# Optimization experiments

Hardware: AMD Instinct MI355X
Metric: run time of the kernel (lower is better)

The kernel has to match this reference:

```python
import jax, jax.numpy as jnp
import numpy as np

B, S, D, H = 2, 2048, 1024, 16
DK = D // H  # 64
THETA = 10000.0


def setup_inputs() -> dict:
    key = jax.random.key(0)
    ks = jax.random.split(key, 5)
    scale = 1.0 / np.sqrt(D)
    return {
        "x": jax.random.normal(ks[0], (B, S, D), dtype=jnp.float32),
        "Wq": jax.random.normal(ks[1], (D, D), dtype=jnp.float32) * scale,
        "Wk": jax.random.normal(ks[2], (D, D), dtype=jnp.float32) * scale,
        "Wv": jax.random.normal(ks[3], (D, D), dtype=jnp.float32) * scale,
        "Wo": jax.random.normal(ks[4], (D, D), dtype=jnp.float32) * scale,
    }


def _rope(t):
    # t: (B, H, S, DK); interleaved-pair rotary embedding with positions 0..S-1
    s = t.shape[-2]
    inv_freq = 1.0 / (THETA ** (jnp.arange(0, DK, 2, dtype=jnp.float32) / DK))  # (DK/2,)
    ang = jnp.arange(s, dtype=jnp.float32)[:, None] * inv_freq[None, :]  # (S, DK/2)
    cos, sin = jnp.cos(ang), jnp.sin(ang)
    x1 = t[..., 0::2]
    x2 = t[..., 1::2]
    r1 = x1 * cos - x2 * sin
    r2 = x1 * sin + x2 * cos
    return jnp.stack([r1, r2], axis=-1).reshape(t.shape)


def reference(x, Wq, Wk, Wv, Wo):
    # Projections (Linear: y = x @ W^T), split heads -> (B, H, S, DK)
    def proj(W):
        y = jnp.einsum('bsd,ed->bse', x, W)
        return y.reshape(B, S, H, DK).transpose(0, 2, 1, 3)

    Q = _rope(proj(Wq))
    K = _rope(proj(Wk))
    V = proj(Wv)

    scores = jnp.einsum('bhqd,bhkd->bhqk', Q, K)
    scores = jnp.clip(scores, -80.0, 80.0)
    causal = jnp.tril(jnp.ones((S, S), dtype=bool))  # (S, S)
    scores = jnp.where(causal, scores, -jnp.inf)
    weights = jax.nn.softmax(scores / np.sqrt(DK), axis=-1)
    att = jnp.einsum('bhqk,bhkd->bhqd', weights, V)
    att = att.transpose(0, 2, 1, 3).reshape(B, S, D)
    return jnp.einsum('bsd,ed->bse', att, Wo)
```

## Files before the change

### kernel.cpp

```cpp
#include <hip/hip_runtime.h>
#include <hip/hip_bf16.h>

#define B_  2
#define S_  2048
#define D_  1024
#define H_  16
#define DK_ 64
#define BH_ (B_*H_)
#define M_  (B_*S_)

typedef __attribute__((ext_vector_type(8))) short bf16x8;
typedef __attribute__((ext_vector_type(4))) float f32x4;

__device__ inline float bf2f(unsigned short u) {
    return __uint_as_float(((unsigned)u) << 16);
}
__device__ inline unsigned short f2bf(float f) {
    unsigned u = __float_as_uint(f);
    u += 0x7fffu + ((u >> 16) & 1u);
    return (unsigned short)(u >> 16);
}
__device__ inline unsigned short f2bf_hw(float f) {
    __hip_bfloat16 h = __float2bfloat16(f);
    return *reinterpret_cast<unsigned short*>(&h);
}
__device__ inline unsigned packbf2(float lo, float hi) {
    return (unsigned)f2bf_hw(lo) | ((unsigned)f2bf_hw(hi) << 16);
}

__device__ inline void gld16(const void* g, void* l) {
    __builtin_amdgcn_global_load_lds(
        (const __attribute__((address_space(1))) unsigned int*)g,
        (__attribute__((address_space(3))) unsigned int*)l, 16, 0, 0);
}

__global__ void cast_f32_to_bf16(const float* __restrict__ src,
                                 unsigned short* __restrict__ dst, int n) {
    int i = (blockIdx.x * blockDim.x + threadIdx.x) * 4;
    int stride = gridDim.x * blockDim.x * 4;
    for (int j = i; j < n; j += stride) {
        float4 v = *reinterpret_cast<const float4*>(src + j);
        ushort4 o;
        o.x = f2bf(v.x); o.y = f2bf(v.y); o.z = f2bf(v.z); o.w = f2bf(v.w);
        *reinterpret_cast<ushort4*>(dst + j) = o;
    }
}

__global__ void cast4_f32_to_bf16(const float* __restrict__ s0, const float* __restrict__ s1,
                                  const float* __restrict__ s2, const float* __restrict__ s3,
                                  unsigned short* __restrict__ d0, unsigned short* __restrict__ d1,
                                  unsigned short* __restrict__ d2, unsigned short* __restrict__ d3) {
    const float* s; unsigned short* d;
    switch (blockIdx.y) {
        case 0: s = s0; d = d0; break;
        case 1: s = s1; d = d1; break;
        case 2: s = s2; d = d2; break;
        default: s = s3; d = d3; break;
    }
    int j = (blockIdx.x * blockDim.x + threadIdx.x) * 4;
    float4 v = *reinterpret_cast<const float4*>(s + j);
    ushort4 o;
    o.x = f2bf(v.x); o.y = f2bf(v.y); o.z = f2bf(v.z); o.w = f2bf(v.w);
    *reinterpret_cast<ushort4*>(d + j) = o;
}

#define BM 64
#define BN 128
#define BKG 64

__global__ __launch_bounds__(256)
void gemm_qkv(const unsigned short* __restrict__ A, const unsigned short* __restrict__ Wcat,
              unsigned short* __restrict__ Qw, unsigned short* __restrict__ Kw,
              unsigned short* __restrict__ Vt) {
    __shared__ unsigned short As[BM * BKG];
    __shared__ unsigned short Bs[BN * BKG];
    const int K = D_;
    const int tid  = threadIdx.x;
    const int lane = tid & 63;
    const int wid  = tid >> 6;
    const int wm = wid & 1, wn = wid >> 1;
    const int m0 = blockIdx.y * BM, n0 = blockIdx.x * BN;
    const int g  = lane >> 4, cl = lane & 15;

    f32x4 acc[2][4];
#pragma unroll
    for (int i = 0; i < 2; i++)
#pragma unroll
        for (int j = 0; j < 4; j++) acc[i][j] = f32x4{0.f, 0.f, 0.f, 0.f};

    const int srow = tid >> 3;
    const unsigned short* Asrc[2];
    const unsigned short* Bsrc[4];
#pragma unroll
    for (int q = 0; q < 2; q++) {
        int row = srow + q * 32;
        Asrc[q] = A + (long)(m0 + row) * K + (((tid & 7) ^ (row & 7)) * 8);
    }
#pragma unroll
    for (int q = 0; q < 4; q++) {
        int row = srow + q * 32;
        Bsrc[q] = Wcat + (long)(n0 + row) * K + (((tid & 7) ^ (row & 7)) * 8);
    }

    for (int k0 = 0; k0 < K; k0 += BKG) {
        __syncthreads();
#pragma unroll
        for (int q = 0; q < 2; q++) gld16(Asrc[q] + k0, As + tid * 8 + q * 2048);
#pragma unroll
        for (int q = 0; q < 4; q++) gld16(Bsrc[q] + k0, Bs + tid * 8 + q * 2048);
        __syncthreads();

#pragma unroll
        for (int kk = 0; kk < 2; kk++) {
            bf16x8 af[2], bfr[4];
#pragma unroll
            for (int i = 0; i < 2; i++) {
                int row = wm*32 + i*16 + cl;
                af[i]  = *reinterpret_cast<const bf16x8*>(As + row * BKG + (((kk*4 + g) ^ (cl & 7)) * 8));
            }
#pragma unroll
            for (int j = 0; j < 4; j++) {
                int row = wn*64 + j*16 + cl;
                bfr[j] = *reinterpret_cast<const bf16x8*>(Bs + row * BKG + (((kk*4 + g) ^ (cl & 7)) * 8));
            }
#pragma unroll
            for (int i = 0; i < 2; i++)
#pragma unroll
                for (int j = 0; j < 4; j++)
                    acc[i][j] = __builtin_amdgcn_mfma_f32_16x16x32_bf16(af[i], bfr[j], acc[i][j], 0, 0, 0);
        }
    }

    const int mat = n0 >> 10;
    if (mat < 2) {
        unsigned short* dst = mat ? Kw : Qw;
        float invf[4];
#pragma unroll
        for (int jj = 0; jj < 4; jj++)
            invf[jj] = exp2f(-(float)(jj*8 + (cl >> 1)) * 0.4152410118569779f);
#pragma unroll
        for (int i = 0; i < 2; i++) {
#pragma unroll
            for (int jj = 0; jj < 4; jj++) {
                const int gcl = (n0 & 1023) + wn*64 + jj*16 + cl;
                const int hh = gcl >> 6;
                const int dk = jj*16 + cl;
#pragma unroll
                for (int rr = 0; rr < 4; rr++) {
                    int gr = m0 + wm*32 + i*16 + g*4 + rr;
                    int bb = gr >> 11, s = gr & (S_ - 1);
                    float v = acc[i][jj][rr];
                    float p = __shfl_xor(v, 1);
                    float ang = (float)s * invf[jj];
                    float sn = __sinf(ang), cs = __cosf(ang);
                    float r = (cl & 1) ? fmaf(v, cs, p * sn) : fmaf(v, cs, -p * sn);
                    dst[(((long)(bb*H_ + hh) * S_ + s) << 6) + dk] = f2bf_hw(r);
                }
            }
        }
    } else {
#pragma unroll
        for (int i = 0; i < 2; i++) {
#pragma unroll
            for (int jj = 0; jj < 4; jj++) {
                const int gcl = (n0 & 1023) + wn*64 + jj*16 + cl;
                const int hh = gcl >> 6;
                const int dk = jj*16 + cl;
#pragma unroll
                for (int rr = 0; rr < 4; rr++) {
                    int gr = m0 + wm*32 + i*16 + g*4 + rr;
                    int bb = gr >> 11, s = gr & (S_ - 1);
                    Vt[((long)(bb*H_ + hh) * DK_ + dk) * S_ + s] = f2bf_hw(acc[i][jj][rr]);
                }
            }
        }
    }
}

__global__ __launch_bounds__(256)
void gemm_out(const unsigned short* __restrict__ A, const unsigned short* __restrict__ Bw,
              float* __restrict__ Cf) {
    __shared__ unsigned short As[BM * BKG];
    __shared__ unsigned short Bs[BN * BKG];
    const int K = D_;
    const int tid  = threadIdx.x;
    const int lane = tid & 63;
    const int wid  = tid >> 6;
    const int wm = wid & 1, wn = wid >> 1;
    const int m0 = blockIdx.y * BM, n0 = blockIdx.x * BN;
    const int g  = lane >> 4, cl = lane & 15;

    f32x4 acc[2][4];
#pragma unroll
    for (int i = 0; i < 2; i++)
#pragma unroll
        for (int j = 0; j < 4; j++) acc[i][j] = f32x4{0.f, 0.f, 0.f, 0.f};

    const int srow = tid >> 3;
    const unsigned short* Asrc[2];
    const unsigned short* Bsrc[4];
#pragma unroll
    for (int q = 0; q < 2; q++) {
        int row = srow + q * 32;
        Asrc[q] = A + (long)(m0 + row) * K + (((tid & 7) ^ (row & 7)) * 8);
    }
#pragma unroll
    for (int q = 0; q < 4; q++) {
        int row = srow + q * 32;
        Bsrc[q] = Bw + (long)(n0 + row) * K + (((tid & 7) ^ (row & 7)) * 8);
    }

    for (int k0 = 0; k0 < K; k0 += BKG) {
        __syncthreads();
#pragma unroll
        for (int q = 0; q < 2; q++) gld16(Asrc[q] + k0, As + tid * 8 + q * 2048);
#pragma unroll
        for (int q = 0; q < 4; q++) gld16(Bsrc[q] + k0, Bs + tid * 8 + q * 2048);
        __syncthreads();

#pragma unroll
        for (int kk = 0; kk < 2; kk++) {
            bf16x8 af[2], bfr[4];
#pragma unroll
            for (int i = 0; i < 2; i++) {
                int row = wm*32 + i*16 + cl;
                af[i]  = *reinterpret_cast<const bf16x8*>(As + row * BKG + (((kk*4 + g) ^ (cl & 7)) * 8));
            }
#pragma unroll
            for (int j = 0; j < 4; j++) {
                int row = wn*64 + j*16 + cl;
                bfr[j] = *reinterpret_cast<const bf16x8*>(Bs + row * BKG + (((kk*4 + g) ^ (cl & 7)) * 8));
            }
#pragma unroll
            for (int i = 0; i < 2; i++)
#pragma unroll
                for (int j = 0; j < 4; j++)
                    acc[i][j] = __builtin_amdgcn_mfma_f32_16x16x32_bf16(af[i], bfr[j], acc[i][j], 0, 0, 0);
        }
    }

#pragma unroll
    for (int i = 0; i < 2; i++)
#pragma unroll
        for (int j = 0; j < 4; j++)
#pragma unroll
            for (int rr = 0; rr < 4; rr++) {
                int gr = m0 + wm*32 + i*16 + g*4 + rr;
                int gc = n0 + wn*64 + j*16 + cl;
                Cf[(long)gr * D_ + gc] = acc[i][j][rr];
            }
}

#define WQ    32
#define KVBLK 64
#define LDP   72

__global__ __launch_bounds__(256)
void flash_attn(const unsigned short* __restrict__ Qw, const unsigned short* __restrict__ Kw,
                const unsigned short* __restrict__ Vt, unsigned short* __restrict__ Att) {
    __shared__ __align__(16) char smem[20480];
    const int tid  = threadIdx.x;
    const int lane = tid & 63;
    const int wid  = tid >> 6;
    const int g = lane >> 4, cl = lane & 15;
    const int bh = blockIdx.x & (BH_ - 1);
    const int pr = blockIdx.x >> 5;
    const int b = bh >> 4, h = bh & (H_ - 1);

    unsigned short* Ps = reinterpret_cast<unsigned short*>(smem) + wid * (WQ * LDP);
    f32x4* Ol = reinterpret_cast<f32x4*>(smem);
    float* Ll = reinterpret_cast<float*>(smem + 16384);

    const unsigned short* Kb = Kw + (long)bh * S_ * DK_;
    const unsigned short* Vb = Vt + (long)bh * DK_ * S_;

    for (int half = 0; half < 2; half++) {
        const int qt = half ? (S_/WQ - 1 - pr) : pr;
        const int q0 = qt * WQ;
        const int nt = (q0 + WQ + KVBLK - 1) / KVBLK;

        const unsigned short* Qb = Qw + ((long)bh * S_ + q0) * DK_;
        bf16x8 aq[2][2];
#pragma unroll
        for (int m = 0; m < 2; m++)
#pragma unroll
            for (int c = 0; c < 2; c++)
                aq[m][c] = *reinterpret_cast<const bf16x8*>(Qb + (m*16 + cl) * DK_ + c*32 + g*8);

        f32x4 o[2][4];
#pragma unroll
        for (int m = 0; m < 2; m++)
#pragma unroll
            for (int t = 0; t < 4; t++) o[m][t] = f32x4{0.f, 0.f, 0.f, 0.f};
        float lp[2] = {0.f, 0.f};

        for (int j = wid; j < nt; j += 4) {
            const int kv0 = j * KVBLK;
            bf16x8 bk[4][2];
#pragma unroll
            for (int n = 0; n < 4; n++)
#pragma unroll
                for (int c = 0; c < 2; c++)
                    bk[n][c] = *reinterpret_cast<const bf16x8*>(Kb + (long)(kv0 + n*16 + cl) * DK_ + c*32 + g*8);
            f32x4 sc[2][4];
#pragma unroll
            for (int m = 0; m < 2; m++)
#pragma unroll
                for (int n = 0; n < 4; n++) {
                    f32x4 z = f32x4{0.f, 0.f, 0.f, 0.f};
                    z = __builtin_amdgcn_mfma_f32_16x16x32_bf16(bk[n][0], aq[m][0], z, 0, 0, 0);
                    z = __builtin_amdgcn_mfma_f32_16x16x32_bf16(bk[n][1], aq[m][1], z, 0, 0, 0);
                    sc[m][n] = z;
                }

            if (kv0 + KVBLK - 1 > q0) {
#pragma unroll
                for (int m = 0; m < 2; m++) {
                    const int q = q0 + m*16 + cl;
#pragma unroll
                    for (int n = 0; n < 4; n++) {
                        float p4[4];
#pragma unroll
                        for (int rr = 0; rr < 4; rr++) {
                            float u = fminf(fmaf(sc[m][n][rr], 0.125f, -10.f), 0.f);
                            if (kv0 + n*16 + g*4 + rr > q) u = -1e30f;
                            p4[rr] = __expf(u);
                        }
                        lp[m] += (p4[0] + p4[1]) + (p4[2] + p4[3]);
                        *reinterpret_cast<uint2*>(Ps + (m*16 + cl) * LDP + n*16 + g*4)
                            = uint2{packbf2(p4[0], p4[1]), packbf2(p4[2], p4[3])};
                    }
                }
            } else {
#pragma unroll
                for (int m = 0; m < 2; m++) {
#pragma unroll
                    for (int n = 0; n < 4; n++) {
                        float p4[4];
#pragma unroll
                        for (int rr = 0; rr < 4; rr++)
                            p4[rr] = __expf(fminf(fmaf(sc[m][n][rr], 0.125f, -10.f), 0.f));
                        lp[m] += (p4[0] + p4[1]) + (p4[2] + p4[3]);
                        *reinterpret_cast<uint2*>(Ps + (m*16 + cl) * LDP + n*16 + g*4)
                            = uint2{packbf2(p4[0], p4[1]), packbf2(p4[2], p4[3])};
                    }
                }
            }

            bf16x8 pa[2][2];
#pragma unroll
            for (int m = 0; m < 2; m++)
#pragma unroll
                for (int c = 0; c < 2; c++)
                    pa[m][c] = *reinterpret_cast<const bf16x8*>(Ps + (m*16 + cl) * LDP + c*32 + g*8);
            bf16x8 bv[4][2];
#pragma unroll
            for (int t = 0; t < 4; t++)
#pragma unroll
                for (int c = 0; c < 2; c++)
                    bv[t][c] = *reinterpret_cast<const bf16x8*>(Vb + (long)(t*16 + cl) * S_ + kv0 + c*32 + g*8);
#pragma unroll
            for (int m = 0; m < 2; m++)
#pragma unroll
                for (int t = 0; t < 4; t++) {
                    o[m][t] = __builtin_amdgcn_mfma_f32_16x16x32_bf16(pa[m][0], bv[t][0], o[m][t], 0, 0, 0);
                    o[m][t] = __builtin_amdgcn_mfma_f32_16x16x32_bf16(pa[m][1], bv[t][1], o[m][t], 0, 0, 0);
                }
        }

        __syncthreads();
        if (wid == 1 || wid == 3) {
            const int slot = wid >> 1;
#pragma unroll
            for (int m = 0; m < 2; m++) {
#pragma unroll
                for (int t = 0; t < 4; t++)
                    Ol[(slot*8 + m*4 + t)*64 + lane] = o[m][t];
                Ll[(slot*2 + m)*64 + lane] = lp[m];
            }
        }
        __syncthreads();
        if (wid == 0 || wid == 2) {
            const int slot = wid >> 1;
#pragma unroll
            for (int m = 0; m < 2; m++) {
#pragma unroll
                for (int t = 0; t < 4; t++) {
                    f32x4 v = Ol[(slot*8 + m*4 + t)*64 + lane];
#pragma unroll
                    for (int rr = 0; rr < 4; rr++) o[m][t][rr] += v[rr];
                }
                lp[m] += Ll[(slot*2 + m)*64 + lane];
            }
        }
        __syncthreads();
        if (wid == 2) {
#pragma unroll
            for (int m = 0; m < 2; m++) {
#pragma unroll
                for (int t = 0; t < 4; t++)
                    Ol[(m*4 + t)*64 + lane] = o[m][t];
                Ll[m*64 + lane] = lp[m];
            }
        }
        __syncthreads();
        if (wid == 0) {
#pragma unroll
            for (int m = 0; m < 2; m++) {
#pragma unroll
                for (int t = 0; t < 4; t++) {
                    f32x4 v = Ol[(m*4 + t)*64 + lane];
#pragma unroll
                    for (int rr = 0; rr < 4; rr++) o[m][t][rr] += v[rr];
                }
                lp[m] += Ll[m*64 + lane];
                lp[m] += __shfl_xor(lp[m], 16);
                lp[m] += __shfl_xor(lp[m], 32);
            }
            float linv[2][4];
#pragma unroll
            for (int m = 0; m < 2; m++)
#pragma unroll
                for (int rr = 0; rr < 4; rr++)
                    linv[m][rr] = 1.0f / __shfl(lp[m], g*4 + rr);
#pragma unroll
            for (int m = 0; m < 2; m++)
#pragma unroll
                for (int t = 0; t < 4; t++)
#pragma unroll
                    for (int rr = 0; rr < 4; rr++) {
                        const int q = q0 + m*16 + g*4 + rr;
                        const int d = t*16 + cl;
                        Att[(long)(b * S_ + q) * D_ + h * DK_ + d] = f2bf_hw(o[m][t][rr] * linv[m][rr]);
                    }
        }
        __syncthreads();
    }
}

extern "C" void kernel_launch(void* const* d_in, const int* in_sizes, int n_in,
                              void* d_out, int out_size, void* d_ws, size_t ws_size,
                              hipStream_t stream) {
    const float* x  = (const float*)d_in[0];
    const float* Wq = (const float*)d_in[1];
    const float* Wk = (const float*)d_in[2];
    const float* Wv = (const float*)d_in[3];
    const float* Wo = (const float*)d_in[4];
    float* out = (float*)d_out;

    char* ws = (char*)d_ws;
    unsigned short* xb  = (unsigned short*)(ws);
    unsigned short* att = xb;
    unsigned short* WqB = (unsigned short*)(ws + (8  << 20));
    unsigned short* WkB = (unsigned short*)(ws + (10 << 20));
    unsigned short* WvB = (unsigned short*)(ws + (12 << 20));
    unsigned short* WoB = (unsigned short*)(ws + (14 << 20));
    unsigned short* Qw  = (unsigned short*)(ws + (16 << 20));
    unsigned short* Kw  = (unsigned short*)(ws + (24 << 20));
    unsigned short* Vt  = (unsigned short*)(ws + (32 << 20));

    const int nx = B_ * S_ * D_;
    cast_f32_to_bf16<<<4096, 256, 0, stream>>>(x, xb, nx);
    cast4_f32_to_bf16<<<dim3(1024, 4), 256, 0, stream>>>(Wq, Wk, Wv, Wo, WqB, WkB, WvB, WoB);

    dim3 qkvgrid(3 * D_ / BN, M_ / BM);
    gemm_qkv<<<qkvgrid, 256, 0, stream>>>(xb, WqB, Qw, Kw, Vt);

    flash_attn<<<(S_/WQ/2) * BH_, 256, 0, stream>>>(Qw, Kw, Vt, att);

    dim3 ogrid(D_ / BN, M_ / BM);
    gemm_out<<<ogrid, 256, 0, stream>>>(att, WoB, out);
}
```

Before: 144.3 us.

## Store Q/K/V in MFMA fragment-native layout for contiguous attention loads

The QKV GEMM epilogue now writes Q, K and V into a pre-swizzled layout matching the MFMA operand fragment order, so each lane in flash attention loads its 16-byte fragment from a contiguous wave-wide 1KB block. Before, K and Q loads were strided by rows and V loads were strided by S. V stores are also vectorized to ushort4 instead of scalar transposed writes. The cost is more complex index math in the producer and scattered scalar stores for Q/K.

```diff
diff --git a/kernel.cpp b/kernel.cpp
--- a/kernel.cpp
+++ b/kernel.cpp
@@ -70,8 +70,8 @@
 
 __global__ __launch_bounds__(256)
 void gemm_qkv(const unsigned short* __restrict__ A, const unsigned short* __restrict__ Wcat,
-              unsigned short* __restrict__ Qw, unsigned short* __restrict__ Kw,
-              unsigned short* __restrict__ Vt) {
+              unsigned short* __restrict__ Qf, unsigned short* __restrict__ Kf,
+              unsigned short* __restrict__ Vf) {
     __shared__ unsigned short As[BM * BKG];
     __shared__ unsigned short Bs[BN * BKG];
     const int K = D_;
@@ -133,7 +133,7 @@
 
     const int mat = n0 >> 10;
     if (mat < 2) {
-        unsigned short* dst = mat ? Kw : Qw;
+        unsigned short* dst = mat ? Kf : Qf;
         float invf[4];
 #pragma unroll
         for (int jj = 0; jj < 4; jj++)
@@ -145,6 +145,9 @@
                 const int gcl = (n0 & 1023) + wn*64 + jj*16 + cl;
                 const int hh = gcl >> 6;
                 const int dk = jj*16 + cl;
+                const int c  = dk >> 5;
+                const int lsel = ((dk >> 3) & 3) << 4;
+                const int e  = dk & 7;
 #pragma unroll
                 for (int rr = 0; rr < 4; rr++) {
                     int gr = m0 + wm*32 + i*16 + g*4 + rr;
@@ -154,7 +157,10 @@
                     float ang = (float)s * invf[jj];
                     float sn = __sinf(ang), cs = __cosf(ang);
                     float r = (cl & 1) ? fmaf(v, cs, p * sn) : fmaf(v, cs, -p * sn);
-                    dst[(((long)(bb*H_ + hh) * S_ + s) << 6) + dk] = f2bf_hw(r);
+                    const int lane_p = (s & 15) | lsel;
+                    long idx = ((long)(bb*H_ + hh) * 128 + (s >> 4)) * 1024
+                             + c * 512 + lane_p * 8 + e;
+                    dst[idx] = f2bf_hw(r);
                 }
             }
         }
@@ -165,13 +171,16 @@
             for (int jj = 0; jj < 4; jj++) {
                 const int gcl = (n0 & 1023) + wn*64 + jj*16 + cl;
                 const int hh = gcl >> 6;
-                const int dk = jj*16 + cl;
-#pragma unroll
-                for (int rr = 0; rr < 4; rr++) {
-                    int gr = m0 + wm*32 + i*16 + g*4 + rr;
-                    int bb = gr >> 11, s = gr & (S_ - 1);
-                    Vt[((long)(bb*H_ + hh) * DK_ + dk) * S_ + s] = f2bf_hw(acc[i][jj][rr]);
-                }
+                const int sbase = m0 + wm*32 + i*16 + g*4;
+                const int bb = sbase >> 11, s0l = sbase & (S_ - 1);
+                const int lane_p = cl | (((s0l >> 3) & 3) << 4);
+                const int e0 = s0l & 7;
+                ushort4 o;
+                o.x = f2bf_hw(acc[i][jj][0]); o.y = f2bf_hw(acc[i][jj][1]);
+                o.z = f2bf_hw(acc[i][jj][2]); o.w = f2bf_hw(acc[i][jj][3]);
+                long idx = ((long)(bb*H_ + hh) * 4 + jj) * 32768
+                         + (long)(s0l >> 5) * 512 + lane_p * 8 + e0;
+                *reinterpret_cast<ushort4*>(Vf + idx) = o;
             }
         }
     }
@@ -256,8 +265,8 @@
 #define LDP   72
 
 __global__ __launch_bounds__(256)
-void flash_attn(const unsigned short* __restrict__ Qw, const unsigned short* __restrict__ Kw,
-                const unsigned short* __restrict__ Vt, unsigned short* __restrict__ Att) {
+void flash_attn(const unsigned short* __restrict__ Qf, const unsigned short* __restrict__ Kf,
+                const unsigned short* __restrict__ Vf, unsigned short* __restrict__ Att) {
     __shared__ __align__(16) char smem[20480];
     const int tid  = threadIdx.x;
     const int lane = tid & 63;
@@ -271,21 +280,21 @@
     f32x4* Ol = reinterpret_cast<f32x4*>(smem);
     float* Ll = reinterpret_cast<float*>(smem + 16384);
 
-    const unsigned short* Kb = Kw + (long)bh * S_ * DK_;
-    const unsigned short* Vb = Vt + (long)bh * DK_ * S_;
+    const unsigned short* Qb = Qf + (long)bh * 131072;
+    const unsigned short* Kb = Kf + (long)bh * 131072;
+    const unsigned short* Vb = Vf + (long)bh * 131072;
 
     for (int half = 0; half < 2; half++) {
         const int qt = half ? (S_/WQ - 1 - pr) : pr;
         const int q0 = qt * WQ;
         const int nt = (q0 + WQ + KVBLK - 1) / KVBLK;
 
-        const unsigned short* Qb = Qw + ((long)bh * S_ + q0) * DK_;
         bf16x8 aq[2][2];
 #pragma unroll
         for (int m = 0; m < 2; m++)
 #pragma unroll
             for (int c = 0; c < 2; c++)
-                aq[m][c] = *reinterpret_cast<const bf16x8*>(Qb + (m*16 + cl) * DK_ + c*32 + g*8);
+                aq[m][c] = *reinterpret_cast<const bf16x8*>(Qb + ((q0 >> 4) + m) * 1024 + c * 512 + lane * 8);
 
         f32x4 o[2][4];
 #pragma unroll
@@ -301,7 +310,7 @@
             for (int n = 0; n < 4; n++)
 #pragma unroll
                 for (int c = 0; c < 2; c++)
-                    bk[n][c] = *reinterpret_cast<const bf16x8*>(Kb + (long)(kv0 + n*16 + cl) * DK_ + c*32 + g*8);
+                    bk[n][c] = *reinterpret_cast<const bf16x8*>(Kb + ((kv0 >> 4) + n) * 1024 + c * 512 + lane * 8);
             f32x4 sc[2][4];
 #pragma unroll
             for (int m = 0; m < 2; m++)
@@ -358,7 +367,7 @@
             for (int t = 0; t < 4; t++)
 #pragma unroll
                 for (int c = 0; c < 2; c++)
-                    bv[t][c] = *reinterpret_cast<const bf16x8*>(Vb + (long)(t*16 + cl) * S_ + kv0 + c*32 + g*8);
+                    bv[t][c] = *reinterpret_cast<const bf16x8*>(Vb + (long)t * 32768 + ((kv0 >> 5) + c) * 512 + lane * 8);
 #pragma unroll
             for (int m = 0; m < 2; m++)
 #pragma unroll
@@ -455,18 +464,18 @@
     unsigned short* WkB = (unsigned short*)(ws + (10 << 20));
     unsigned short* WvB = (unsigned short*)(ws + (12 << 20));
     unsigned short* WoB = (unsigned short*)(ws + (14 << 20));
-    unsigned short* Qw  = (unsigned short*)(ws + (16 << 20));
-    unsigned short* Kw  = (unsigned short*)(ws + (24 << 20));
-    unsigned short* Vt  = (unsigned short*)(ws + (32 << 20));
+    unsigned short* Qf  = (unsigned short*)(ws + (16 << 20));
+    unsigned short* Kf  = (unsigned short*)(ws + (24 << 20));
+    unsigned short* Vf  = (unsigned short*)(ws + (32 << 20));
 
     const int nx = B_ * S_ * D_;
     cast_f32_to_bf16<<<4096, 256, 0, stream>>>(x, xb, nx);
     cast4_f32_to_bf16<<<dim3(1024, 4), 256, 0, stream>>>(Wq, Wk, Wv, Wo, WqB, WkB, WvB, WoB);
 
     dim3 qkvgrid(3 * D_ / BN, M_ / BM);
-    gemm_qkv<<<qkvgrid, 256, 0, stream>>>(xb, WqB, Qw, Kw, Vt);
-
-    flash_attn<<<(S_/WQ/2) * BH_, 256, 0, stream>>>(Qw, Kw, Vt, att);
+    gemm_qkv<<<qkvgrid, 256, 0, stream>>>(xb, WqB, Qf, Kf, Vf);
+
+    flash_attn<<<(S_/WQ/2) * BH_, 256, 0, stream>>>(Qf, Kf, Vf, att);
 
     dim3 ogrid(D_ / BN, M_ / BM);
     gemm_out<<<ogrid, 256, 0, stream>>>(att, WoB, out);
```

After: 115.8 us. 19.8% less time.
